# Kernel tuning notes

Hardware: AMD Instinct MI355X
Metric: run time of the kernel (lower is better)

The kernel has to match this reference:

```python
import jax, jax.numpy as jnp
import numpy as np
from jax import lax

CENSUS_R = 3
EDGE_WEIGHT = 4.0


def _grayscale(img):
    # ITU-R 601 luma, as in tf.image.rgb_to_grayscale used by UnFlow-style census
    w = jnp.array([0.299, 0.587, 0.114], dtype=img.dtype)
    return jnp.einsum('bchw,c->bhw', img, w)[:, None]  # (B,1,H,W)


def _grid(H, W, dtype):
    gy, gx = jnp.meshgrid(jnp.arange(H, dtype=dtype), jnp.arange(W, dtype=dtype), indexing='ij')
    return gy, gx


def _warp_bilinear(img, flow):
    # Resample2d: out(x,y) = img(x + u, y + v), bilinear, clamped at borders.
    B, C, H, W = img.shape
    gy, gx = _grid(H, W, flow.dtype)
    x = gx[None] + flow[:, 0]   # (B,H,W)
    y = gy[None] + flow[:, 1]
    x0 = jnp.floor(x); y0 = jnp.floor(y)
    wx = (x - x0)[:, None]; wy = (y - y0)[:, None]  # (B,1,H,W)
    x0i = jnp.clip(x0.astype(jnp.int32), 0, W - 1)
    x1i = jnp.clip(x0i + 1, 0, W - 1)
    y0i = jnp.clip(y0.astype(jnp.int32), 0, H - 1)
    y1i = jnp.clip(y0i + 1, 0, H - 1)
    flat = img.reshape(B, C, H * W)

    def gather(yi, xi):
        idx = (yi * W + xi).reshape(B, 1, H * W)
        return jnp.take_along_axis(flat, idx, axis=2).reshape(B, C, H, W)

    return (gather(y0i, x0i) * (1.0 - wx) * (1.0 - wy)
            + gather(y0i, x1i) * wx * (1.0 - wy)
            + gather(y1i, x0i) * (1.0 - wx) * wy
            + gather(y1i, x1i) * wx * wy)


def _border_mask(flow):
    # 1 where the flow target lands inside the image, 0 otherwise. (B,1,H,W)
    B, _, H, W = flow.shape
    gy, gx = _grid(H, W, flow.dtype)
    x = gx[None] + flow[:, 0]
    y = gy[None] + flow[:, 1]
    inside = (x >= 0) & (x <= W - 1) & (y >= 0) & (y <= H - 1)
    return inside[:, None].astype(flow.dtype)


def _charbonnier(x, mask=None, alpha=0.45, eps=1e-3):
    err = (x * x + eps * eps) ** alpha
    if mask is not None:
        err = err * mask
    return jnp.sum(err) / x.size


def _census_transform(img, r):
    gray = _grayscale(img) * 255.0
    p = 2 * r + 1
    # identity kernel extracts the (2r+1)^2 neighborhood per pixel
    k = jnp.asarray(np.eye(p * p, dtype=np.float32).reshape(p * p, 1, p, p))
    patches = lax.conv_general_dilated(gray, k, (1, 1), 'SAME',
                                       dimension_numbers=('NCHW', 'OIHW', 'NCHW'))
    d = patches - gray  # (B,p*p,H,W)
    return d / jnp.sqrt(0.81 + d * d)


def _census_loss(img1, img2_warp, mask, r):
    t1 = _census_transform(img1, r)
    t2 = _census_transform(img2_warp, r)
    dist = (t1 - t2) ** 2
    dist = dist / (0.1 + dist)                 # soft hamming per neighbor
    dist = jnp.sum(dist, axis=1, keepdims=True)  # (B,1,H,W)
    B, _, H, W = img1.shape
    inner = jnp.zeros((1, 1, H, W), img1.dtype).at[:, :, r:H - r, r:W - r].set(1.0)
    return _charbonnier(dist, mask * inner)


def _smooth_grad_1st(flow, img, edge_weight):
    img_dx = img[:, :, :, :-1] - img[:, :, :, 1:]
    img_dy = img[:, :, :-1, :] - img[:, :, 1:, :]
    w_x = jnp.exp(-jnp.mean(jnp.abs(img_dx), axis=1, keepdims=True) * edge_weight)
    w_y = jnp.exp(-jnp.mean(jnp.abs(img_dy), axis=1, keepdims=True) * edge_weight)
    f_dx = flow[:, :, :, :-1] - flow[:, :, :, 1:]
    f_dy = flow[:, :, :-1, :] - flow[:, :, 1:, :]
    pen = lambda d: (d * d + 1e-6) ** 0.45  # charbonnier penalty
    return 0.5 * (jnp.mean(w_x * pen(f_dx)) + jnp.mean(w_y * pen(f_dy)))


def setup_inputs() -> dict:
    key = jax.random.key(0)
    k1, k2, k3, k4 = jax.random.split(key, 4)
    B, H, W = 8, 448, 1024
    return {
        'flow1': jax.random.normal(k1, (B, 2, H, W), dtype=jnp.float32),
        'target1': jax.random.normal(k2, (B, 2, H, W), dtype=jnp.float32),
        'input1': jax.random.uniform(k3, (B, 3, H, W), dtype=jnp.float32),
        'input2': jax.random.uniform(k4, (B, 3, H, W), dtype=jnp.float32),
    }


def reference(flow1, target1, input1, input2):
    mask = _border_mask(flow1)
    img2_warp = _warp_bilinear(input2, flow1)
    census = 1.0 * _census_loss(input1, img2_warp, mask, CENSUS_R)
    smooth = 1.0 * _smooth_grad_1st(flow1, input1, EDGE_WEIGHT)
    energy = census + smooth
    epe = jnp.mean(jnp.sqrt(jnp.sum((flow1 - target1) ** 2, axis=1)))
    return (energy, epe)
```

## Files before the change

### kernel.cpp

```cpp
#include <hip/hip_runtime.h>
#include <math.h>

#define BB 8
#define HH 448
#define WW 1024
#define HWSZ (HH*WW)
#define NPIX (BB*HH*WW)
#define CR 3
#define TX 64
#define TY 16
#define HX (TX+2*CR)
#define HXP 72
#define HY (TY+2*CR)
#define NBX 16
#define NBY 28
#define NB  (NBX*NBY*BB)

__device__ __forceinline__ float pen45(float dd) {
    return __expf(0.45f * __logf(dd));
}

__device__ __forceinline__ float gray3(float r, float g, float b) {
    return (0.299f * r + 0.587f * g + 0.114f * b) * 255.0f;
}


__global__ __launch_bounds__(256) void k_fused(
    const float* __restrict__ flow, const float* __restrict__ target,
    const float* __restrict__ img1, const float* __restrict__ img2,
    float* __restrict__ part)
{
    __shared__ float t1s[HY][HXP];
    __shared__ float t2s[HY][HXP];
    __shared__ float fus[HY][HXP];
    __shared__ float fvs[HY][HXP];

    const int b  = blockIdx.z;
    const int x0 = blockIdx.x * TX;
    const int y0 = blockIdx.y * TY;
    const int tid = threadIdx.x;

    const float* i1r = img1 + (size_t)b * 3 * HWSZ;
    const float* i1g = i1r + HWSZ;
    const float* i1b = i1r + 2 * HWSZ;
    const float* i2r = img2 + (size_t)b * 3 * HWSZ;
    const float* i2g = i2r + HWSZ;
    const float* i2b = i2r + 2 * HWSZ;
    const float* fu  = flow + (size_t)b * 2 * HWSZ;
    const float* fv  = fu + HWSZ;
    const float* tu  = target + (size_t)b * 2 * HWSZ;
    const float* tv  = tu + HWSZ;

    for (int i = tid; i < HY * HX; i += 256) {
        int ly = i / HX, lx = i - ly * HX;
        int gx = x0 - CR + lx; gx = gx < 0 ? 0 : (gx > WW - 1 ? WW - 1 : gx);
        int gy = y0 - CR + ly; gy = gy < 0 ? 0 : (gy > HH - 1 ? HH - 1 : gy);
        int gidx = gy * WW + gx;
        t1s[ly][lx] = gray3(i1r[gidx], i1g[gidx], i1b[gidx]);
        float u = fu[gidx], v = fv[gidx];
        fus[ly][lx] = u; fvs[ly][lx] = v;
        float xx = (float)gx + u, yy = (float)gy + v;
        float fx = floorf(xx), fy = floorf(yy);
        float wx = xx - fx, wy = yy - fy;
        int xi0 = (int)fx; xi0 = xi0 < 0 ? 0 : (xi0 > WW - 1 ? WW - 1 : xi0);
        int xi1 = xi0 + 1 > WW - 1 ? WW - 1 : xi0 + 1;
        int yi0 = (int)fy; yi0 = yi0 < 0 ? 0 : (yi0 > HH - 1 ? HH - 1 : yi0);
        int yi1 = yi0 + 1 > HH - 1 ? HH - 1 : yi0 + 1;
        int i00 = yi0 * WW + xi0, i01 = yi0 * WW + xi1;
        int i10 = yi1 * WW + xi0, i11 = yi1 * WW + xi1;
        float g00 = gray3(i2r[i00], i2g[i00], i2b[i00]);
        float g01 = gray3(i2r[i01], i2g[i01], i2b[i01]);
        float g10 = gray3(i2r[i10], i2g[i10], i2b[i10]);
        float g11 = gray3(i2r[i11], i2g[i11], i2b[i11]);
        t2s[ly][lx] = g00 * ((1.0f - wx) * (1.0f - wy)) + g01 * (wx * (1.0f - wy))
                    + g10 * ((1.0f - wx) * wy) + g11 * (wx * wy);
    }
    __syncthreads();

    const int txg = tid & 15;
    const int ty  = tid >> 4;
    const int lxb = txg * 4;
    const int rowc = ty + CR;

    float dist[4] = {0.f, 0.f, 0.f, 0.f};
    float c1[4], c2[4];

#define LOADROW(ROW, V1, V2)                                            \
    float V1[12], V2[12];                                               \
    {                                                                   \
        float4 _a0 = *(const float4*)&t1s[ROW][lxb];                    \
        float4 _a1 = *(const float4*)&t1s[ROW][lxb + 4];                \
        float4 _a2 = *(const float4*)&t1s[ROW][lxb + 8];                \
        float4 _b0 = *(const float4*)&t2s[ROW][lxb];                    \
        float4 _b1 = *(const float4*)&t2s[ROW][lxb + 4];                \
        float4 _b2 = *(const float4*)&t2s[ROW][lxb + 8];                \
        V1[0]=_a0.x; V1[1]=_a0.y; V1[2]=_a0.z; V1[3]=_a0.w;             \
        V1[4]=_a1.x; V1[5]=_a1.y; V1[6]=_a1.z; V1[7]=_a1.w;             \
        V1[8]=_a2.x; V1[9]=_a2.y; V1[10]=_a2.z; V1[11]=_a2.w;           \
        V2[0]=_b0.x; V2[1]=_b0.y; V2[2]=_b0.z; V2[3]=_b0.w;             \
        V2[4]=_b1.x; V2[5]=_b1.y; V2[6]=_b1.z; V2[7]=_b1.w;             \
        V2[8]=_b2.x; V2[9]=_b2.y; V2[10]=_b2.z; V2[11]=_b2.w;           \
    }

#define PAIR(V1, V2, K, DX)                                              \
    {                                                                    \
        float _d1 = V1[3 + (K) + (DX)] - c1[K];                          \
        float _d2 = V2[3 + (K) + (DX)] - c2[K];                          \
        float _u1 = _d1 * __builtin_amdgcn_rsqf(fmaf(_d1, _d1, 0.81f));  \
        float _u2 = _d2 * __builtin_amdgcn_rsqf(fmaf(_d2, _d2, 0.81f));  \
        float _dd = _u1 - _u2;                                           \
        float _s = _dd * _dd;                                            \
        dist[K] = fmaf(_s, __builtin_amdgcn_rcpf(0.1f + _s), dist[K]);   \
    }

    {
        LOADROW(rowc, v1, v2)
        #pragma unroll
        for (int k = 0; k < 4; k++) { c1[k] = v1[3 + k]; c2[k] = v2[3 + k]; }
        #pragma unroll
        for (int k = 0; k < 4; k++) {
            #pragma unroll
            for (int dx = -CR; dx <= CR; dx++) {
                if (dx == 0) continue;
                PAIR(v1, v2, k, dx)
            }
        }
    }
    #pragma unroll
    for (int dyi = 0; dyi < 6; dyi++) {
        const int dy = (dyi < 3) ? (dyi - 3) : (dyi - 2);
        const int row = rowc + dy;
        LOADROW(row, v1, v2)
        #pragma unroll
        for (int k = 0; k < 4; k++) {
            #pragma unroll
            for (int dx = -CR; dx <= CR; dx++) {
                PAIR(v1, v2, k, dx)
            }
        }
    }
#undef LOADROW
#undef PAIR

    const int cy = y0 + ty;
    const int cxb = x0 + lxb;

    float s_cen = 0.0f;
    #pragma unroll
    for (int k = 0; k < 4; k++) {
        const int cx = cxb + k;
        const bool validc = (cx >= CR) && (cx <= WW - 1 - CR) && (cy >= CR) && (cy <= HH - 1 - CR);
        float u = fus[rowc][lxb + CR + k], v = fvs[rowc][lxb + CR + k];
        float xx = (float)cx + u, yy = (float)cy + v;
        const bool inside = (xx >= 0.0f) && (xx <= (float)(WW - 1)) &&
                            (yy >= 0.0f) && (yy <= (float)(HH - 1));
        if (validc && inside) s_cen += pen45(fmaf(dist[k], dist[k], 1e-6f));
    }

    const int gidx  = cy * WW + cxb;
    const int xnext = (cxb + 4 > WW - 1) ? (WW - 1) : (cxb + 4);
    const int gidxn = cy * WW + xnext;
    const int ydn   = (cy + 1 > HH - 1) ? (HH - 1) : (cy + 1);
    const int gidxd = ydn * WW + cxb;

    float4 r4 = *(const float4*)(i1r + gidx);
    float4 g4 = *(const float4*)(i1g + gidx);
    float4 b4 = *(const float4*)(i1b + gidx);
    float rn = i1r[gidxn], gn = i1g[gidxn], bn = i1b[gidxn];
    float4 u4 = *(const float4*)(fu + gidx);
    float4 v4 = *(const float4*)(fv + gidx);
    float un = fu[gidxn], vn = fv[gidxn];
    float4 tu4 = *(const float4*)(tu + gidx);
    float4 tv4 = *(const float4*)(tv + gidx);

    float R[5] = {r4.x, r4.y, r4.z, r4.w, rn};
    float G[5] = {g4.x, g4.y, g4.z, g4.w, gn};
    float Bc[5] = {b4.x, b4.y, b4.z, b4.w, bn};
    float U[5] = {u4.x, u4.y, u4.z, u4.w, un};
    float V[5] = {v4.x, v4.y, v4.z, v4.w, vn};
    float TU[4] = {tu4.x, tu4.y, tu4.z, tu4.w};
    float TV[4] = {tv4.x, tv4.y, tv4.z, tv4.w};

    float s_ep = 0.0f, s_sx = 0.0f, s_sy = 0.0f;
    #pragma unroll
    for (int k = 0; k < 4; k++) {
        float du = U[k] - TU[k], dv = V[k] - TV[k];
        s_ep += sqrtf(du * du + dv * dv);
        if (cxb + k < WW - 1) {
            float ad = fabsf(R[k] - R[k+1]) + fabsf(G[k] - G[k+1]) + fabsf(Bc[k] - Bc[k+1]);
            float wx = __expf(-(4.0f / 3.0f) * ad);
            float d0 = U[k] - U[k+1], d1 = V[k] - V[k+1];
            s_sx += wx * (pen45(fmaf(d0, d0, 1e-6f)) + pen45(fmaf(d1, d1, 1e-6f)));
        }
    }

    if (cy < HH - 1) {
        float4 rd = *(const float4*)(i1r + gidxd);
        float4 gd = *(const float4*)(i1g + gidxd);
        float4 bd = *(const float4*)(i1b + gidxd);
        float4 ud = *(const float4*)(fu + gidxd);
        float4 vd = *(const float4*)(fv + gidxd);
        float RD[4] = {rd.x, rd.y, rd.z, rd.w};
        float GD[4] = {gd.x, gd.y, gd.z, gd.w};
        float BD[4] = {bd.x, bd.y, bd.z, bd.w};
        float UD[4] = {ud.x, ud.y, ud.z, ud.w};
        float VD[4] = {vd.x, vd.y, vd.z, vd.w};
        #pragma unroll
        for (int k = 0; k < 4; k++) {
            float ad = fabsf(R[k] - RD[k]) + fabsf(G[k] - GD[k]) + fabsf(Bc[k] - BD[k]);
            float wy = __expf(-(4.0f / 3.0f) * ad);
            float d0 = U[k] - UD[k], d1 = V[k] - VD[k];
            s_sy += wy * (pen45(fmaf(d0, d0, 1e-6f)) + pen45(fmaf(d1, d1, 1e-6f)));
        }
    }

    #pragma unroll
    for (int off = 32; off; off >>= 1) {
        s_cen += __shfl_down(s_cen, off);
        s_sx  += __shfl_down(s_sx, off);
        s_sy  += __shfl_down(s_sy, off);
        s_ep  += __shfl_down(s_ep, off);
    }
    __shared__ float red[4][4];
    const int lane = tid & 63, wid = tid >> 6;
    if (lane == 0) { red[0][wid] = s_cen; red[1][wid] = s_sx; red[2][wid] = s_sy; red[3][wid] = s_ep; }
    __syncthreads();
    if (tid == 0) {
        const int bid = (b * NBY + blockIdx.y) * NBX + blockIdx.x;
        part[bid]           = red[0][0] + red[0][1] + red[0][2] + red[0][3];
        part[NB + bid]      = red[1][0] + red[1][1] + red[1][2] + red[1][3];
        part[2 * NB + bid]  = red[2][0] + red[2][1] + red[2][2] + red[2][3];
        part[3 * NB + bid]  = red[3][0] + red[3][1] + red[3][2] + red[3][3];
    }
}

__global__ __launch_bounds__(256) void k_final(
    const float* __restrict__ part, float* __restrict__ out)
{
    const int tid = threadIdx.x;
    float cn = 0.f, sx = 0.f, sy = 0.f, ep = 0.f;
    for (int i = tid; i < NB; i += 256) {
        cn += part[i];
        sx += part[NB + i];
        sy += part[2 * NB + i];
        ep += part[3 * NB + i];
    }
    #pragma unroll
    for (int off = 32; off; off >>= 1) {
        cn += __shfl_down(cn, off); sx += __shfl_down(sx, off);
        sy += __shfl_down(sy, off); ep += __shfl_down(ep, off);
    }
    __shared__ float r[4][4];
    const int lane = tid & 63, wid = tid >> 6;
    if (lane == 0) { r[0][wid] = cn; r[1][wid] = sx; r[2][wid] = sy; r[3][wid] = ep; }
    __syncthreads();
    if (tid == 0) {
        cn = r[0][0] + r[0][1] + r[0][2] + r[0][3];
        sx = r[1][0] + r[1][1] + r[1][2] + r[1][3];
        sy = r[2][0] + r[2][1] + r[2][2] + r[2][3];
        ep = r[3][0] + r[3][1] + r[3][2] + r[3][3];
        float census = cn / (float)NPIX;
        float mx = sx / (float)((size_t)BB * 2 * HH * (WW - 1));
        float my = sy / (float)((size_t)BB * 2 * (HH - 1) * WW);
        out[0] = census + 0.5f * (mx + my);
        out[1] = ep / (float)NPIX;
    }
}

extern "C" void kernel_launch(void* const* d_in, const int* in_sizes, int n_in,
                              void* d_out, int out_size, void* d_ws, size_t ws_size,
                              hipStream_t stream) {
    const float* flow   = (const float*)d_in[0];
    const float* target = (const float*)d_in[1];
    const float* img1   = (const float*)d_in[2];
    const float* img2   = (const float*)d_in[3];
    float* out  = (float*)d_out;
    float* part = (float*)d_ws;

    dim3 gr(NBX, NBY, BB);
    k_fused<<<gr, dim3(256, 1, 1), 0, stream>>>(flow, target, img1, img2, part);
    k_final<<<1, dim3(256, 1, 1), 0, stream>>>(part, out);
}
```

Baseline: 295.8 us.

## Precompute img2 grayscale in a separate pass and drop flow shared tiles

A new kernel converts img2 to a single grayscale plane in workspace, so the bilinear warp gathers four scalars per pixel instead of twelve channel values. The flow shared-memory tiles are removed and the border mask is computed from flow values held in registers. The smoothness and EPE loads are moved ahead of the census loop, the shared-memory row pitch is padded from 72 to 76, and launch bounds now request 6 blocks per SM. The cost is an extra kernel launch plus a write and re-read of a full grayscale image through global memory, and the tighter launch bound may cause register spills.

```diff
diff --git a/kernel.cpp b/kernel.cpp
--- a/kernel.cpp
+++ b/kernel.cpp
@@ -10,7 +10,7 @@
 #define TX 64
 #define TY 16
 #define HX (TX+2*CR)
-#define HXP 72
+#define HXP 76
 #define HY (TY+2*CR)
 #define NBX 16
 #define NBY 28
@@ -25,15 +25,32 @@
 }
 
 
-__global__ __launch_bounds__(256) void k_fused(
+__global__ __launch_bounds__(256) void k_g2gray(
+    const float* __restrict__ img2, float* __restrict__ g2)
+{
+    const int tid = threadIdx.x;
+    const int y = blockIdx.x;
+    const int b = blockIdx.y;
+    const int idx = y * WW + tid * 4;
+    const float* i2r = img2 + (size_t)b * 3 * HWSZ;
+    float4 r = *(const float4*)(i2r + idx);
+    float4 g = *(const float4*)(i2r + HWSZ + idx);
+    float4 bl = *(const float4*)(i2r + 2 * HWSZ + idx);
+    float4 o;
+    o.x = gray3(r.x, g.x, bl.x);
+    o.y = gray3(r.y, g.y, bl.y);
+    o.z = gray3(r.z, g.z, bl.z);
+    o.w = gray3(r.w, g.w, bl.w);
+    *(float4*)(g2 + (size_t)b * HWSZ + idx) = o;
+}
+
+__global__ __launch_bounds__(256, 6) void k_fused(
     const float* __restrict__ flow, const float* __restrict__ target,
-    const float* __restrict__ img1, const float* __restrict__ img2,
+    const float* __restrict__ img1, const float* __restrict__ g2,
     float* __restrict__ part)
 {
     __shared__ float t1s[HY][HXP];
     __shared__ float t2s[HY][HXP];
-    __shared__ float fus[HY][HXP];
-    __shared__ float fvs[HY][HXP];
 
     const int b  = blockIdx.z;
     const int x0 = blockIdx.x * TX;
@@ -43,9 +60,7 @@
     const float* i1r = img1 + (size_t)b * 3 * HWSZ;
     const float* i1g = i1r + HWSZ;
     const float* i1b = i1r + 2 * HWSZ;
-    const float* i2r = img2 + (size_t)b * 3 * HWSZ;
-    const float* i2g = i2r + HWSZ;
-    const float* i2b = i2r + 2 * HWSZ;
+    const float* g2b = g2 + (size_t)b * HWSZ;
     const float* fu  = flow + (size_t)b * 2 * HWSZ;
     const float* fv  = fu + HWSZ;
     const float* tu  = target + (size_t)b * 2 * HWSZ;
@@ -58,7 +73,6 @@
         int gidx = gy * WW + gx;
         t1s[ly][lx] = gray3(i1r[gidx], i1g[gidx], i1b[gidx]);
         float u = fu[gidx], v = fv[gidx];
-        fus[ly][lx] = u; fvs[ly][lx] = v;
         float xx = (float)gx + u, yy = (float)gy + v;
         float fx = floorf(xx), fy = floorf(yy);
         float wx = xx - fx, wy = yy - fy;
@@ -66,12 +80,8 @@
         int xi1 = xi0 + 1 > WW - 1 ? WW - 1 : xi0 + 1;
         int yi0 = (int)fy; yi0 = yi0 < 0 ? 0 : (yi0 > HH - 1 ? HH - 1 : yi0);
         int yi1 = yi0 + 1 > HH - 1 ? HH - 1 : yi0 + 1;
-        int i00 = yi0 * WW + xi0, i01 = yi0 * WW + xi1;
-        int i10 = yi1 * WW + xi0, i11 = yi1 * WW + xi1;
-        float g00 = gray3(i2r[i00], i2g[i00], i2b[i00]);
-        float g01 = gray3(i2r[i01], i2g[i01], i2b[i01]);
-        float g10 = gray3(i2r[i10], i2g[i10], i2b[i10]);
-        float g11 = gray3(i2r[i11], i2g[i11], i2b[i11]);
+        float g00 = g2b[yi0 * WW + xi0], g01 = g2b[yi0 * WW + xi1];
+        float g10 = g2b[yi1 * WW + xi0], g11 = g2b[yi1 * WW + xi1];
         t2s[ly][lx] = g00 * ((1.0f - wx) * (1.0f - wy)) + g01 * (wx * (1.0f - wy))
                     + g10 * ((1.0f - wx) * wy) + g11 * (wx * wy);
     }
@@ -81,6 +91,68 @@
     const int ty  = tid >> 4;
     const int lxb = txg * 4;
     const int rowc = ty + CR;
+    const int cy = y0 + ty;
+    const int cxb = x0 + lxb;
+
+    const int gidx  = cy * WW + cxb;
+    const int xnext = (cxb + 4 > WW - 1) ? (WW - 1) : (cxb + 4);
+    const int gidxn = cy * WW + xnext;
+    const int ydn   = (cy + 1 > HH - 1) ? (HH - 1) : (cy + 1);
+    const int gidxd = ydn * WW + cxb;
+
+    float4 u4 = *(const float4*)(fu + gidx);
+    float4 v4 = *(const float4*)(fv + gidx);
+    float U[5] = {u4.x, u4.y, u4.z, u4.w, fu[gidxn]};
+    float V[5] = {v4.x, v4.y, v4.z, v4.w, fv[gidxn]};
+
+    float s_ep = 0.0f, s_sx = 0.0f, s_sy = 0.0f;
+    float msk[4];
+    {
+        float4 tu4 = *(const float4*)(tu + gidx);
+        float4 tv4 = *(const float4*)(tv + gidx);
+        float TU[4] = {tu4.x, tu4.y, tu4.z, tu4.w};
+        float TV[4] = {tv4.x, tv4.y, tv4.z, tv4.w};
+        float4 r4 = *(const float4*)(i1r + gidx);
+        float4 g4 = *(const float4*)(i1g + gidx);
+        float4 b4 = *(const float4*)(i1b + gidx);
+        float R[5] = {r4.x, r4.y, r4.z, r4.w, i1r[gidxn]};
+        float G[5] = {g4.x, g4.y, g4.z, g4.w, i1g[gidxn]};
+        float Bc[5] = {b4.x, b4.y, b4.z, b4.w, i1b[gidxn]};
+
+        #pragma unroll
+        for (int k = 0; k < 4; k++) {
+            float du = U[k] - TU[k], dv = V[k] - TV[k];
+            s_ep += sqrtf(du * du + dv * dv);
+            float xx = (float)(cxb + k) + U[k], yy = (float)cy + V[k];
+            msk[k] = ((xx >= 0.0f) && (xx <= (float)(WW - 1)) &&
+                      (yy >= 0.0f) && (yy <= (float)(HH - 1))) ? 1.0f : 0.0f;
+            if (cxb + k < WW - 1) {
+                float ad = fabsf(R[k] - R[k+1]) + fabsf(G[k] - G[k+1]) + fabsf(Bc[k] - Bc[k+1]);
+                float wx = __expf(-(4.0f / 3.0f) * ad);
+                float d0 = U[k] - U[k+1], d1 = V[k] - V[k+1];
+                s_sx += wx * (pen45(fmaf(d0, d0, 1e-6f)) + pen45(fmaf(d1, d1, 1e-6f)));
+            }
+        }
+        if (cy < HH - 1) {
+            float4 rd = *(const float4*)(i1r + gidxd);
+            float4 gd = *(const float4*)(i1g + gidxd);
+            float4 bd = *(const float4*)(i1b + gidxd);
+            float4 ud = *(const float4*)(fu + gidxd);
+            float4 vd = *(const float4*)(fv + gidxd);
+            float RD[4] = {rd.x, rd.y, rd.z, rd.w};
+            float GD[4] = {gd.x, gd.y, gd.z, gd.w};
+            float BD[4] = {bd.x, bd.y, bd.z, bd.w};
+            float UD[4] = {ud.x, ud.y, ud.z, ud.w};
+            float VD[4] = {vd.x, vd.y, vd.z, vd.w};
+            #pragma unroll
+            for (int k = 0; k < 4; k++) {
+                float ad = fabsf(R[k] - RD[k]) + fabsf(G[k] - GD[k]) + fabsf(Bc[k] - BD[k]);
+                float wy = __expf(-(4.0f / 3.0f) * ad);
+                float d0 = U[k] - UD[k], d1 = V[k] - VD[k];
+                s_sy += wy * (pen45(fmaf(d0, d0, 1e-6f)) + pen45(fmaf(d1, d1, 1e-6f)));
+            }
+        }
+    }
 
     float dist[4] = {0.f, 0.f, 0.f, 0.f};
     float c1[4], c2[4];
@@ -142,76 +214,12 @@
 #undef LOADROW
 #undef PAIR
 
-    const int cy = y0 + ty;
-    const int cxb = x0 + lxb;
-
     float s_cen = 0.0f;
     #pragma unroll
     for (int k = 0; k < 4; k++) {
         const int cx = cxb + k;
         const bool validc = (cx >= CR) && (cx <= WW - 1 - CR) && (cy >= CR) && (cy <= HH - 1 - CR);
-        float u = fus[rowc][lxb + CR + k], v = fvs[rowc][lxb + CR + k];
-        float xx = (float)cx + u, yy = (float)cy + v;
-        const bool inside = (xx >= 0.0f) && (xx <= (float)(WW - 1)) &&
-                            (yy >= 0.0f) && (yy <= (float)(HH - 1));
-        if (validc && inside) s_cen += pen45(fmaf(dist[k], dist[k], 1e-6f));
-    }
-
-    const int gidx  = cy * WW + cxb;
-    const int xnext = (cxb + 4 > WW - 1) ? (WW - 1) : (cxb + 4);
-    const int gidxn = cy * WW + xnext;
-    const int ydn   = (cy + 1 > HH - 1) ? (HH - 1) : (cy + 1);
-    const int gidxd = ydn * WW + cxb;
-
-    float4 r4 = *(const float4*)(i1r + gidx);
-    float4 g4 = *(const float4*)(i1g + gidx);
-    float4 b4 = *(const float4*)(i1b + gidx);
-    float rn = i1r[gidxn], gn = i1g[gidxn], bn = i1b[gidxn];
-    float4 u4 = *(const float4*)(fu + gidx);
-    float4 v4 = *(const float4*)(fv + gidx);
-    float un = fu[gidxn], vn = fv[gidxn];
-    float4 tu4 = *(const float4*)(tu + gidx);
-    float4 tv4 = *(const float4*)(tv + gidx);
-
-    float R[5] = {r4.x, r4.y, r4.z, r4.w, rn};
-    float G[5] = {g4.x, g4.y, g4.z, g4.w, gn};
-    float Bc[5] = {b4.x, b4.y, b4.z, b4.w, bn};
-    float U[5] = {u4.x, u4.y, u4.z, u4.w, un};
-    float V[5] = {v4.x, v4.y, v4.z, v4.w, vn};
-    float TU[4] = {tu4.x, tu4.y, tu4.z, tu4.w};
-    float TV[4] = {tv4.x, tv4.y, tv4.z, tv4.w};
-
-    float s_ep = 0.0f, s_sx = 0.0f, s_sy = 0.0f;
-    #pragma unroll
-    for (int k = 0; k < 4; k++) {
-        float du = U[k] - TU[k], dv = V[k] - TV[k];
-        s_ep += sqrtf(du * du + dv * dv);
-        if (cxb + k < WW - 1) {
-            float ad = fabsf(R[k] - R[k+1]) + fabsf(G[k] - G[k+1]) + fabsf(Bc[k] - Bc[k+1]);
-            float wx = __expf(-(4.0f / 3.0f) * ad);
-            float d0 = U[k] - U[k+1], d1 = V[k] - V[k+1];
-            s_sx += wx * (pen45(fmaf(d0, d0, 1e-6f)) + pen45(fmaf(d1, d1, 1e-6f)));
-        }
-    }
-
-    if (cy < HH - 1) {
-        float4 rd = *(const float4*)(i1r + gidxd);
-        float4 gd = *(const float4*)(i1g + gidxd);
-        float4 bd = *(const float4*)(i1b + gidxd);
-        float4 ud = *(const float4*)(fu + gidxd);
-        float4 vd = *(const float4*)(fv + gidxd);
-        float RD[4] = {rd.x, rd.y, rd.z, rd.w};
-        float GD[4] = {gd.x, gd.y, gd.z, gd.w};
-        float BD[4] = {bd.x, bd.y, bd.z, bd.w};
-        float UD[4] = {ud.x, ud.y, ud.z, ud.w};
-        float VD[4] = {vd.x, vd.y, vd.z, vd.w};
-        #pragma unroll
-        for (int k = 0; k < 4; k++) {
-            float ad = fabsf(R[k] - RD[k]) + fabsf(G[k] - GD[k]) + fabsf(Bc[k] - BD[k]);
-            float wy = __expf(-(4.0f / 3.0f) * ad);
-            float d0 = U[k] - UD[k], d1 = V[k] - VD[k];
-            s_sy += wy * (pen45(fmaf(d0, d0, 1e-6f)) + pen45(fmaf(d1, d1, 1e-6f)));
-        }
+        if (validc) s_cen += msk[k] * pen45(fmaf(dist[k], dist[k], 1e-6f));
     }
 
     #pragma unroll
@@ -276,8 +284,12 @@
     const float* img2   = (const float*)d_in[3];
     float* out  = (float*)d_out;
     float* part = (float*)d_ws;
+    float* g2   = (float*)((char*)d_ws + 65536);
+
+    dim3 grg(HH, BB, 1);
+    k_g2gray<<<grg, dim3(256, 1, 1), 0, stream>>>(img2, g2);
 
     dim3 gr(NBX, NBY, BB);
-    k_fused<<<gr, dim3(256, 1, 1), 0, stream>>>(flow, target, img1, img2, part);
+    k_fused<<<gr, dim3(256, 1, 1), 0, stream>>>(flow, target, img1, g2, part);
     k_final<<<1, dim3(256, 1, 1), 0, stream>>>(part, out);
 }
```

New measurement: 432.9 us. +46.4%, slower.
